# Performance work log

Hardware: AMD Instinct MI355X
Metric: run time of the kernel (lower is better)

## Reference

```python
import jax, jax.numpy as jnp
import numpy as np

B, S_IMG, S_TXT, D, H, HD, R = 1, 1536, 512, 3072, 24, 128, 32
INNER = H * HD  # 3072
EPS = 1e-5


def svdq_linear(x, W, down, up, b=None):
    # Float reference of SVDQW4A4Linear: quantized base GEMM + SVD low-rank branch.
    y = x @ W.T + (x @ down) @ up
    if b is not None:
        y = y + b
    return y


def rms_norm(x, w):
    # RMSNorm over last dim (dim_head)
    var = jnp.mean(x * x, axis=-1, keepdims=True)
    return x * jax.lax.rsqrt(var + EPS) * w


def apply_rope(x, cos, sin):
    # x: (B, S, H, HD); cos/sin: (S, HD//2), interleaved complex rotation
    b, s, h, d = x.shape
    xr = x.reshape(b, s, h, d // 2, 2)
    x0, x1 = xr[..., 0], xr[..., 1]
    c = cos[None, :, None, :]
    sn = sin[None, :, None, :]
    o0 = x0 * c - x1 * sn
    o1 = x0 * sn + x1 * c
    return jnp.stack([o0, o1], axis=-1).reshape(b, s, h, d)


def setup_inputs() -> dict:
    key = jax.random.key(0)
    ks = jax.random.split(key, 24)
    sc = 0.02
    inp = {
        'hidden_states': jax.random.normal(ks[0], (B, S_IMG, D), jnp.float32),
        'encoder_hidden_states': jax.random.normal(ks[1], (B, S_TXT, D), jnp.float32),
    }
    S = S_IMG + S_TXT
    theta = jax.random.uniform(ks[2], (S, HD // 2), jnp.float32, 0.0, 2.0 * np.pi)
    inp['rope_cos'] = jnp.cos(theta)
    inp['rope_sin'] = jnp.sin(theta)
    inp['qkv_w'] = jax.random.normal(ks[3], (3 * INNER, D), jnp.float32) * sc
    inp['qkv_down'] = jax.random.normal(ks[4], (D, R), jnp.float32) * sc
    inp['qkv_up'] = jax.random.normal(ks[5], (R, 3 * INNER), jnp.float32) * sc
    inp['add_qkv_w'] = jax.random.normal(ks[6], (3 * INNER, D), jnp.float32) * sc
    inp['add_qkv_down'] = jax.random.normal(ks[7], (D, R), jnp.float32) * sc
    inp['add_qkv_up'] = jax.random.normal(ks[8], (R, 3 * INNER), jnp.float32) * sc
    inp['out_w'] = jax.random.normal(ks[9], (D, INNER), jnp.float32) * sc
    inp['out_down'] = jax.random.normal(ks[10], (INNER, R), jnp.float32) * sc
    inp['out_up'] = jax.random.normal(ks[11], (R, D), jnp.float32) * sc
    inp['out_b'] = jnp.zeros((D,), jnp.float32)
    inp['add_out_w'] = jax.random.normal(ks[12], (D, INNER), jnp.float32) * sc
    inp['add_out_down'] = jax.random.normal(ks[13], (INNER, R), jnp.float32) * sc
    inp['add_out_up'] = jax.random.normal(ks[14], (R, D), jnp.float32) * sc
    inp['add_out_b'] = jnp.zeros((D,), jnp.float32)
    inp['norm_q_w'] = jnp.ones((HD,), jnp.float32)
    inp['norm_k_w'] = jnp.ones((HD,), jnp.float32)
    inp['norm_added_q_w'] = jnp.ones((HD,), jnp.float32)
    inp['norm_added_k_w'] = jnp.ones((HD,), jnp.float32)
    return inp


def reference(hidden_states, encoder_hidden_states, rope_cos, rope_sin,
              qkv_w, qkv_down, qkv_up,
              add_qkv_w, add_qkv_down, add_qkv_up,
              out_w, out_down, out_up, out_b,
              add_out_w, add_out_down, add_out_up, add_out_b,
              norm_q_w, norm_k_w, norm_added_q_w, norm_added_k_w):
    seq_txt = encoder_hidden_states.shape[1]

    img_qkv = svdq_linear(hidden_states, qkv_w, qkv_down, qkv_up)
    img_q, img_k, img_v = jnp.split(img_qkv, 3, axis=-1)
    txt_qkv = svdq_linear(encoder_hidden_states, add_qkv_w, add_qkv_down, add_qkv_up)
    txt_q, txt_k, txt_v = jnp.split(txt_qkv, 3, axis=-1)

    def heads(x):
        return x.reshape(x.shape[0], x.shape[1], H, HD)

    img_q, img_k, img_v = heads(img_q), heads(img_k), heads(img_v)
    txt_q, txt_k, txt_v = heads(txt_q), heads(txt_k), heads(txt_v)

    img_q = rms_norm(img_q, norm_q_w)
    img_k = rms_norm(img_k, norm_k_w)
    txt_q = rms_norm(txt_q, norm_added_q_w)
    txt_k = rms_norm(txt_k, norm_added_k_w)

    q = jnp.concatenate([txt_q, img_q], axis=1)  # (B, S, H, HD)
    k = jnp.concatenate([txt_k, img_k], axis=1)
    v = jnp.concatenate([txt_v, img_v], axis=1)

    q = apply_rope(q, rope_cos, rope_sin)
    k = apply_rope(k, rope_cos, rope_sin)

    scale = 1.0 / jnp.sqrt(jnp.asarray(HD, q.dtype))
    scores = jnp.einsum('bqhd,bkhd->bhqk', q, k) * scale
    probs = jax.nn.softmax(scores, axis=-1)
    attn = jnp.einsum('bhqk,bkhd->bqhd', probs, v)
    attn = attn.reshape(attn.shape[0], attn.shape[1], INNER)

    txt_attn = attn[:, :seq_txt, :]
    img_attn = attn[:, seq_txt:, :]

    img_out = svdq_linear(img_attn, out_w, out_down, out_up, out_b)
    txt_out = svdq_linear(txt_attn, add_out_w, add_out_down, add_out_up, add_out_b)
    return (img_out, txt_out)
```

## Files before the change

kernel.cpp:

```cpp
#include <hip/hip_runtime.h>
#include <hip/hip_bf16.h>
#include <stdint.h>

typedef __hip_bfloat16 bf16;
typedef __attribute__((ext_vector_type(8))) short short8;
typedef __attribute__((ext_vector_type(4))) short short4b;
typedef __attribute__((ext_vector_type(4))) float floatx4;

__device__ __forceinline__ short bfs(float x) {
    uint32_t u = __builtin_bit_cast(uint32_t, x);
    u += 0x7FFFu + ((u >> 16) & 1u);
    return (short)(u >> 16);
}
__device__ __forceinline__ float b2f(bf16 x) { return __bfloat162float(x); }

__device__ __forceinline__ void load_lds16(const bf16* g, bf16* l) {
    __builtin_amdgcn_global_load_lds(
        (const __attribute__((address_space(1))) uint32_t*)g,
        (__attribute__((address_space(3))) uint32_t*)l, 16, 0, 0);
}

__global__ __launch_bounds__(256) void cvt_bf16(const float* __restrict__ X,
                                                bf16* __restrict__ Y) {
    const size_t i = ((size_t)blockIdx.x * 256 + threadIdx.x) * 8;
    const float4 v0 = *(const float4*)(X + i);
    const float4 v1 = *(const float4*)(X + i + 4);
    short8 o = { bfs(v0.x), bfs(v0.y), bfs(v0.z), bfs(v0.w),
                 bfs(v1.x), bfs(v1.y), bfs(v1.z), bfs(v1.w) };
    *(short8*)(Y + i) = o;
}

__global__ __launch_bounds__(64) void transposeR(const float* __restrict__ U,
                                                 bf16* __restrict__ UT, int N) {
    const int n = blockIdx.x * 64 + threadIdx.x;
    #pragma unroll
    for (int r = 0; r < 32; ++r)
        UT[(size_t)n * 32 + r] = __float2bfloat16(U[(size_t)r * N + n]);
}

__global__ __launch_bounds__(256) void downproj(const bf16* __restrict__ X,
                                                const float* __restrict__ Dn,
                                                bf16* __restrict__ T, int K) {
    const int m = blockIdx.x;
    const int n = threadIdx.x & 31;
    const int kg = threadIdx.x >> 5;
    const bf16* x = X + (size_t)m * K;
    const int kc = K >> 3;
    float acc = 0.f;
    #pragma unroll 4
    for (int k = kg * kc; k < (kg + 1) * kc; ++k)
        acc += b2f(x[k]) * Dn[(size_t)k * 32 + n];
    __shared__ float red[8][32];
    red[kg][n] = acc;
    __syncthreads();
    if (threadIdx.x < 32) {
        float s = 0.f;
        #pragma unroll
        for (int g = 0; g < 8; ++g) s += red[g][n];
        T[(size_t)m * 32 + n] = __float2bfloat16(s);
    }
}

__global__ __launch_bounds__(256) void gemm128(
    const bf16* __restrict__ A, const bf16* __restrict__ B,
    const bf16* __restrict__ T, const bf16* __restrict__ UpT,
    const float* __restrict__ bias, float* __restrict__ C,
    bf16* __restrict__ Qb, bf16* __restrict__ Kb, bf16* __restrict__ Vb,
    int M, int N, int K, int s_base, int mode)
{
    __shared__ __align__(16) bf16 As[128 * 32];
    __shared__ __align__(16) bf16 Bs[128 * 32];
    const int tid = threadIdx.x;
    const int lane = tid & 63, w = tid >> 6;
    const int wm = (w >> 1) * 64, wn = (w & 1) * 64;
    const int lr = lane & 15, lq = lane >> 4;

    int bid = blockIdx.y * gridDim.x + blockIdx.x;
    const int cpx = (gridDim.x * gridDim.y) >> 3;
    bid = (bid & 7) * cpx + (bid >> 3);
    const int by = bid / gridDim.x, bx = bid - by * gridDim.x;
    const int m0 = by * 128, n0 = bx * 128;

    floatx4 acc[4][4] = {};
    const int ksteps = K >> 5;
    for (int kt = 0; kt <= ksteps; ++kt) {
        const bf16 *a_src, *b_src;
        int lda, ldb;
        if (kt < ksteps) {
            a_src = A + (size_t)m0 * K + kt * 32; lda = K;
            b_src = B + (size_t)n0 * K + kt * 32; ldb = K;
        } else {
            a_src = T   + (size_t)m0 * 32; lda = 32;
            b_src = UpT + (size_t)n0 * 32; ldb = 32;
        }
        __syncthreads();
        #pragma unroll
        for (int it = 0; it < 2; ++it) {
            const int c = tid + it * 256;
            const int row = c >> 2, sub = c & 3;
            load_lds16(a_src + (size_t)row * lda + sub * 8, As + c * 8);
        }
        #pragma unroll
        for (int it = 0; it < 2; ++it) {
            const int c = tid + it * 256;
            const int row = c >> 2, sub = c & 3;
            load_lds16(b_src + (size_t)row * ldb + sub * 8, Bs + c * 8);
        }
        __syncthreads();
        short8 af[4], bfr[4];
        #pragma unroll
        for (int i = 0; i < 4; ++i)
            af[i] = *(const short8*)(As + (wm + i * 16 + lr) * 32 + lq * 8);
        #pragma unroll
        for (int j = 0; j < 4; ++j)
            bfr[j] = *(const short8*)(Bs + (wn + j * 16 + lr) * 32 + lq * 8);
        #pragma unroll
        for (int i = 0; i < 4; ++i)
            #pragma unroll
            for (int j = 0; j < 4; ++j)
                acc[i][j] = __builtin_amdgcn_mfma_f32_16x16x32_bf16(
                    af[i], bfr[j], acc[i][j], 0, 0, 0);
    }

    if (mode == 0) {
        #pragma unroll
        for (int j = 0; j < 4; ++j) {
            const int col = n0 + wn + j * 16 + lr;
            const float bv = bias ? bias[col] : 0.0f;
            #pragma unroll
            for (int i = 0; i < 4; ++i) {
                const int rowb = m0 + wm + i * 16 + lq * 4;
                #pragma unroll
                for (int r = 0; r < 4; ++r)
                    C[(size_t)(rowb + r) * N + col] = acc[i][j][r] + bv;
            }
        }
    } else {
        #pragma unroll
        for (int j = 0; j < 4; ++j) {
            const int col = n0 + wn + j * 16 + lr;
            const int which = col / 3072;
            const int cc = col - which * 3072;
            const int hh = cc >> 7, dd = cc & 127;
            #pragma unroll
            for (int i = 0; i < 4; ++i) {
                const int rowb = m0 + wm + i * 16 + lq * 4;
                const int s0 = s_base + rowb;
                if (which == 2) {
                    short4b pv = { bfs(acc[i][j][0]), bfs(acc[i][j][1]),
                                   bfs(acc[i][j][2]), bfs(acc[i][j][3]) };
                    *(short4b*)(Vb + ((size_t)hh * 128 + dd) * 2048 + s0) = pv;
                } else {
                    bf16* dst = (which == 0 ? Qb : Kb)
                              + ((size_t)hh * 2048 + s0) * 128 + dd;
                    #pragma unroll
                    for (int r = 0; r < 4; ++r)
                        dst[(size_t)r * 128] = __float2bfloat16(acc[i][j][r]);
                }
            }
        }
    }
}

__global__ __launch_bounds__(64) void rmsrope(
    bf16* __restrict__ Qb, bf16* __restrict__ Kb,
    const float* __restrict__ cosb, const float* __restrict__ sinb,
    const float* __restrict__ nqw, const float* __restrict__ nkw,
    const float* __restrict__ naqw, const float* __restrict__ nakw)
{
    const int s = blockIdx.x & 2047;
    const int h = blockIdx.x >> 11;
    const int i = threadIdx.x;
    const float c  = cosb[s * 64 + i];
    const float sn = sinb[s * 64 + i];
    const bool txt = (s < 512);
    const size_t base = ((size_t)h * 2048 + s) * 128;

    {
        __hip_bfloat162* row = (__hip_bfloat162*)(Qb + base);
        __hip_bfloat162 pv = row[i];
        float x0 = b2f(pv.x), x1 = b2f(pv.y);
        float ss = x0 * x0 + x1 * x1;
        #pragma unroll
        for (int m = 1; m < 64; m <<= 1) ss += __shfl_xor(ss, m);
        const float rms = rsqrtf(ss * (1.0f / 128.0f) + 1e-5f);
        const float* nw = txt ? naqw : nqw;
        const float y0 = x0 * rms * nw[2 * i];
        const float y1 = x1 * rms * nw[2 * i + 1];
        __hip_bfloat162 o;
        o.x = __float2bfloat16(y0 * c - y1 * sn);
        o.y = __float2bfloat16(y0 * sn + y1 * c);
        row[i] = o;
    }
    {
        __hip_bfloat162* row = (__hip_bfloat162*)(Kb + base);
        __hip_bfloat162 pv = row[i];
        float x0 = b2f(pv.x), x1 = b2f(pv.y);
        float ss = x0 * x0 + x1 * x1;
        #pragma unroll
        for (int m = 1; m < 64; m <<= 1) ss += __shfl_xor(ss, m);
        const float rms = rsqrtf(ss * (1.0f / 128.0f) + 1e-5f);
        const float* nw = txt ? nakw : nkw;
        const float y0 = x0 * rms * nw[2 * i];
        const float y1 = x1 * rms * nw[2 * i + 1];
        __hip_bfloat162 o;
        o.x = __float2bfloat16(y0 * c - y1 * sn);
        o.y = __float2bfloat16(y0 * sn + y1 * c);
        row[i] = o;
    }
}

__global__ __launch_bounds__(256) void attn64(
    const bf16* __restrict__ Qb, const bf16* __restrict__ Kb,
    const bf16* __restrict__ Vb, bf16* __restrict__ attnb)
{
    __shared__ __align__(16) bf16 Ks[64 * 128];
    __shared__ __align__(16) bf16 VsT[128 * 64];
    __shared__ __align__(16) bf16 Ps[4][16 * 64];
    const int tid = threadIdx.x, lane = tid & 63, w = tid >> 6;
    const int lr = lane & 15, lq = lane >> 4;
    const int h = blockIdx.y, q0 = blockIdx.x * 64;
    const float scale = 0.08838834764831845f;

    const bf16* qrow = Qb + ((size_t)h * 2048 + q0 + w * 16 + lr) * 128;
    short8 qf[4];
    #pragma unroll
    for (int ks = 0; ks < 4; ++ks)
        qf[ks] = *(const short8*)(qrow + ks * 32 + lq * 8);

    floatx4 oacc[8] = {};
    float mrow[4] = {-1e30f, -1e30f, -1e30f, -1e30f};
    float lrow[4] = {0.f, 0.f, 0.f, 0.f};

    for (int kt = 0; kt < 32; ++kt) {
        const int kv0 = kt * 64;
        __syncthreads();
        #pragma unroll
        for (int it = 0; it < 4; ++it) {
            const int c = tid + it * 256;
            const int row = c >> 4, cg = (c & 15) ^ (row & 7);
            load_lds16(Kb + ((size_t)h * 2048 + kv0 + row) * 128 + cg * 8,
                       Ks + c * 8);
        }
        #pragma unroll
        for (int it = 0; it < 4; ++it) {
            const int c = tid + it * 256;
            const int row = c >> 3, cg = (c & 7) ^ (row & 7);
            load_lds16(Vb + ((size_t)h * 128 + row) * 2048 + kv0 + cg * 8,
                       VsT + c * 8);
        }
        __syncthreads();

        floatx4 sacc[4] = {};
        __builtin_amdgcn_s_setprio(1);
        #pragma unroll
        for (int ks = 0; ks < 4; ++ks)
            #pragma unroll
            for (int jt = 0; jt < 4; ++jt) {
                const int row = jt * 16 + lr;
                short8 kf = *(const short8*)(
                    Ks + row * 128 + (((ks * 4 + lq) ^ (row & 7)) * 8));
                sacc[jt] = __builtin_amdgcn_mfma_f32_16x16x32_bf16(qf[ks], kf, sacc[jt], 0, 0, 0);
            }
        __builtin_amdgcn_s_setprio(0);

        float alpha_r[4];
        #pragma unroll
        for (int r = 0; r < 4; ++r) {
            float s0 = sacc[0][r] * scale, s1 = sacc[1][r] * scale;
            float s2 = sacc[2][r] * scale, s3 = sacc[3][r] * scale;
            float mx = fmaxf(fmaxf(s0, s1), fmaxf(s2, s3));
            #pragma unroll
            for (int msk = 1; msk < 16; msk <<= 1)
                mx = fmaxf(mx, __shfl_xor(mx, msk));
            const float mn = fmaxf(mrow[r], mx);
            const float al = __expf(mrow[r] - mn);
            s0 = __expf(s0 - mn); s1 = __expf(s1 - mn);
            s2 = __expf(s2 - mn); s3 = __expf(s3 - mn);
            float sum = s0 + s1 + s2 + s3;
            #pragma unroll
            for (int msk = 1; msk < 16; msk <<= 1)
                sum += __shfl_xor(sum, msk);
            lrow[r] = lrow[r] * al + sum;
            mrow[r] = mn;
            alpha_r[r] = al;
            sacc[0][r] = s0; sacc[1][r] = s1; sacc[2][r] = s2; sacc[3][r] = s3;
        }
        #pragma unroll
        for (int nt = 0; nt < 8; ++nt)
            #pragma unroll
            for (int r = 0; r < 4; ++r) oacc[nt][r] *= alpha_r[r];

        #pragma unroll
        for (int jt = 0; jt < 4; ++jt)
            #pragma unroll
            for (int r = 0; r < 4; ++r) {
                const int q = lq * 4 + r;
                const int ir = jt * 16 + lr;
                Ps[w][q * 64 + ((((ir >> 3) ^ (q & 7))) << 3) + (ir & 7)] =
                    __float2bfloat16(sacc[jt][r]);
            }

        short8 pf[2];
        #pragma unroll
        for (int k2 = 0; k2 < 2; ++k2)
            pf[k2] = *(const short8*)(
                &Ps[w][lr * 64 + (((k2 * 4 + lq) ^ (lr & 7)) << 3)]);
        __builtin_amdgcn_s_setprio(1);
        #pragma unroll
        for (int k2 = 0; k2 < 2; ++k2)
            #pragma unroll
            for (int nt = 0; nt < 8; ++nt) {
                const int row = nt * 16 + lr;
                short8 vf = *(const short8*)(
                    VsT + row * 64 + (((k2 * 4 + lq) ^ (row & 7)) * 8));
                oacc[nt] = __builtin_amdgcn_mfma_f32_16x16x32_bf16(pf[k2], vf, oacc[nt], 0, 0, 0);
            }
        __builtin_amdgcn_s_setprio(0);
    }

    float rl[4];
    #pragma unroll
    for (int r = 0; r < 4; ++r) rl[r] = 1.0f / lrow[r];
    #pragma unroll
    for (int nt = 0; nt < 8; ++nt) {
        const int col = h * 128 + nt * 16 + lr;
        #pragma unroll
        for (int r = 0; r < 4; ++r) {
            const int s = q0 + w * 16 + lq * 4 + r;
            attnb[(size_t)s * 3072 + col] = __float2bfloat16(oacc[nt][r] * rl[r]);
        }
    }
}

extern "C" void kernel_launch(void* const* d_in, const int* in_sizes, int n_in,
                              void* d_out, int out_size, void* d_ws, size_t ws_size,
                              hipStream_t stream)
{
    (void)in_sizes; (void)n_in; (void)out_size; (void)ws_size;
    const float* hs        = (const float*)d_in[0];
    const float* ehs       = (const float*)d_in[1];
    const float* rc        = (const float*)d_in[2];
    const float* rs        = (const float*)d_in[3];
    const float* qkv_w     = (const float*)d_in[4];
    const float* qkv_down  = (const float*)d_in[5];
    const float* qkv_up    = (const float*)d_in[6];
    const float* aqkv_w    = (const float*)d_in[7];
    const float* aqkv_down = (const float*)d_in[8];
    const float* aqkv_up   = (const float*)d_in[9];
    const float* out_w     = (const float*)d_in[10];
    const float* out_down  = (const float*)d_in[11];
    const float* out_up    = (const float*)d_in[12];
    const float* out_b     = (const float*)d_in[13];
    const float* aout_w    = (const float*)d_in[14];
    const float* aout_down = (const float*)d_in[15];
    const float* aout_up   = (const float*)d_in[16];
    const float* aout_b    = (const float*)d_in[17];
    const float* nqw  = (const float*)d_in[18];
    const float* nkw  = (const float*)d_in[19];
    const float* naqw = (const float*)d_in[20];
    const float* nakw = (const float*)d_in[21];

    char* ws = (char*)d_ws;
    size_t o = 0;
    bf16* Qb = (bf16*)(ws + o); o += (size_t)24 * 2048 * 128 * 2;
    bf16* Kb = (bf16*)(ws + o); o += (size_t)24 * 2048 * 128 * 2;
    bf16* Vb = (bf16*)(ws + o); o += (size_t)24 * 2048 * 128 * 2;
    bf16* attnb = (bf16*)(ws + o); o += (size_t)2048 * 3072 * 2;
    bf16* Xbi = (bf16*)(ws + o); o += (size_t)1536 * 3072 * 2;
    bf16* Xbt = (bf16*)(ws + o); o += (size_t)512 * 3072 * 2;
    bf16* Wq  = (bf16*)(ws + o); o += (size_t)9216 * 3072 * 2;
    bf16* Waq = (bf16*)(ws + o); o += (size_t)9216 * 3072 * 2;
    bf16* Wo  = Wq;
    bf16* Wao = Wq + (size_t)3072 * 3072;
    bf16* t_img  = (bf16*)(ws + o); o += (size_t)1536 * 32 * 2;
    bf16* t_txt  = (bf16*)(ws + o); o += (size_t)512 * 32 * 2;
    bf16* t2_img = (bf16*)(ws + o); o += (size_t)1536 * 32 * 2;
    bf16* t2_txt = (bf16*)(ws + o); o += (size_t)512 * 32 * 2;
    bf16* upTq  = (bf16*)(ws + o); o += (size_t)9216 * 32 * 2;
    bf16* upTaq = (bf16*)(ws + o); o += (size_t)9216 * 32 * 2;
    bf16* upTo  = (bf16*)(ws + o); o += (size_t)3072 * 32 * 2;
    bf16* upTao = (bf16*)(ws + o); o += (size_t)3072 * 32 * 2;

    cvt_bf16<<<2304, 256, 0, stream>>>(hs, Xbi);
    cvt_bf16<<<768, 256, 0, stream>>>(ehs, Xbt);
    cvt_bf16<<<13824, 256, 0, stream>>>(qkv_w, Wq);
    cvt_bf16<<<13824, 256, 0, stream>>>(aqkv_w, Waq);

    transposeR<<<144, 64, 0, stream>>>(qkv_up, upTq, 9216);
    transposeR<<<144, 64, 0, stream>>>(aqkv_up, upTaq, 9216);
    transposeR<<<48, 64, 0, stream>>>(out_up, upTo, 3072);
    transposeR<<<48, 64, 0, stream>>>(aout_up, upTao, 3072);
    downproj<<<1536, 256, 0, stream>>>(Xbi, qkv_down, t_img, 3072);
    downproj<<<512, 256, 0, stream>>>(Xbt, aqkv_down, t_txt, 3072);

    gemm128<<<dim3(72, 12), 256, 0, stream>>>(Xbi, Wq, t_img, upTq,
        nullptr, nullptr, Qb, Kb, Vb, 1536, 9216, 3072, 512, 1);
    gemm128<<<dim3(72, 4), 256, 0, stream>>>(Xbt, Waq, t_txt, upTaq,
        nullptr, nullptr, Qb, Kb, Vb, 512, 9216, 3072, 0, 1);

    cvt_bf16<<<4608, 256, 0, stream>>>(out_w, Wo);
    cvt_bf16<<<4608, 256, 0, stream>>>(aout_w, Wao);

    rmsrope<<<24 * 2048, 64, 0, stream>>>(Qb, Kb, rc, rs, nqw, nkw, naqw, nakw);

    attn64<<<dim3(32, 24), 256, 0, stream>>>(Qb, Kb, Vb, attnb);

    downproj<<<1536, 256, 0, stream>>>(attnb + (size_t)512 * 3072, out_down, t2_img, 3072);
    downproj<<<512, 256, 0, stream>>>(attnb, aout_down, t2_txt, 3072);

    float* outp = (float*)d_out;
    gemm128<<<dim3(24, 12), 256, 0, stream>>>(attnb + (size_t)512 * 3072, Wo,
        t2_img, upTo, out_b, outp, nullptr, nullptr, nullptr,
        1536, 3072, 3072, 0, 0);
    gemm128<<<dim3(24, 4), 256, 0, stream>>>(attnb, Wao,
        t2_txt, upTao, aout_b, outp + (size_t)1536 * 3072, nullptr, nullptr, nullptr,
        512, 3072, 3072, 0, 0);
}
```

Baseline: 1.104 ms.

## Double-buffer GEMM LDS tiles, merge img/txt GEMM launches, batch rmsrope rows

The GEMM kernel gets two LDS buffers so the global-to-LDS load of the next K step is issued before the MFMAs on the current one, with one barrier per step instead of two. The image and text projections now run as a single grouped launch, with each block picking its operand set by M-tile index, which removes a launch and the tail of the smaller grid. rmsrope packs four rows per 256-thread block and reads the norm weights as float2. The cost is twice the LDS per GEMM block and more pointer-select logic.

Measured after the change: 953.9 us. 1.16x faster.

```diff
diff --git a/kernel.cpp b/kernel.cpp
--- a/kernel.cpp
+++ b/kernel.cpp
@@ -62,14 +62,17 @@
 }
 
 __global__ __launch_bounds__(256) void gemm128(
-    const bf16* __restrict__ A, const bf16* __restrict__ B,
-    const bf16* __restrict__ T, const bf16* __restrict__ UpT,
-    const float* __restrict__ bias, float* __restrict__ C,
+    const bf16* __restrict__ A0, const bf16* __restrict__ B0,
+    const bf16* __restrict__ T0, const bf16* __restrict__ U0,
+    const bf16* __restrict__ A1, const bf16* __restrict__ B1,
+    const bf16* __restrict__ T1, const bf16* __restrict__ U1,
+    const float* __restrict__ bias0, const float* __restrict__ bias1,
+    float* __restrict__ C0, float* __restrict__ C1,
     bf16* __restrict__ Qb, bf16* __restrict__ Kb, bf16* __restrict__ Vb,
-    int M, int N, int K, int s_base, int mode)
+    int mtiles0, int N, int K, int sb0, int sb1, int mode)
 {
-    __shared__ __align__(16) bf16 As[128 * 32];
-    __shared__ __align__(16) bf16 Bs[128 * 32];
+    __shared__ __align__(16) bf16 As[2][128 * 32];
+    __shared__ __align__(16) bf16 Bs[2][128 * 32];
     const int tid = threadIdx.x;
     const int lane = tid & 63, w = tid >> 6;
     const int wm = (w >> 1) * 64, wn = (w & 1) * 64;
@@ -79,60 +82,82 @@
     const int cpx = (gridDim.x * gridDim.y) >> 3;
     bid = (bid & 7) * cpx + (bid >> 3);
     const int by = bid / gridDim.x, bx = bid - by * gridDim.x;
-    const int m0 = by * 128, n0 = bx * 128;
-
-    floatx4 acc[4][4] = {};
+
+    const bool set1 = (by >= mtiles0);
+    const int lby = set1 ? (by - mtiles0) : by;
+    const int m0 = lby * 128, n0 = bx * 128;
+    const bf16* Asel = set1 ? A1 : A0;
+    const bf16* Bsel = set1 ? B1 : B0;
+    const bf16* Tsel = set1 ? T1 : T0;
+    const bf16* Usel = set1 ? U1 : U0;
+    const int s_base = set1 ? sb1 : sb0;
+
     const int ksteps = K >> 5;
-    for (int kt = 0; kt <= ksteps; ++kt) {
+
+    auto stage = [&](int buf, int kt) {
         const bf16 *a_src, *b_src;
         int lda, ldb;
         if (kt < ksteps) {
-            a_src = A + (size_t)m0 * K + kt * 32; lda = K;
-            b_src = B + (size_t)n0 * K + kt * 32; ldb = K;
+            a_src = Asel + (size_t)m0 * K + kt * 32; lda = K;
+            b_src = Bsel + (size_t)n0 * K + kt * 32; ldb = K;
         } else {
-            a_src = T   + (size_t)m0 * 32; lda = 32;
-            b_src = UpT + (size_t)n0 * 32; ldb = 32;
-        }
-        __syncthreads();
+            a_src = Tsel + (size_t)m0 * 32; lda = 32;
+            b_src = Usel + (size_t)n0 * 32; ldb = 32;
+        }
+        bf16* Ad = &As[buf][0];
+        bf16* Bd = &Bs[buf][0];
         #pragma unroll
         for (int it = 0; it < 2; ++it) {
             const int c = tid + it * 256;
             const int row = c >> 2, sub = c & 3;
-            load_lds16(a_src + (size_t)row * lda + sub * 8, As + c * 8);
+            load_lds16(a_src + (size_t)row * lda + sub * 8, Ad + c * 8);
         }
         #pragma unroll
         for (int it = 0; it < 2; ++it) {
             const int c = tid + it * 256;
             const int row = c >> 2, sub = c & 3;
-            load_lds16(b_src + (size_t)row * ldb + sub * 8, Bs + c * 8);
-        }
-        __syncthreads();
+            load_lds16(b_src + (size_t)row * ldb + sub * 8, Bd + c * 8);
+        }
+    };
+
+    floatx4 acc[4][4] = {};
+    stage(0, 0);
+    __syncthreads();
+    int cur = 0;
+    for (int kt = 0; kt <= ksteps; ++kt) {
+        if (kt < ksteps) stage(cur ^ 1, kt + 1);
+        const bf16* Ac = &As[cur][0];
+        const bf16* Bc = &Bs[cur][0];
         short8 af[4], bfr[4];
         #pragma unroll
         for (int i = 0; i < 4; ++i)
-            af[i] = *(const short8*)(As + (wm + i * 16 + lr) * 32 + lq * 8);
+            af[i] = *(const short8*)(Ac + (wm + i * 16 + lr) * 32 + lq * 8);
         #pragma unroll
         for (int j = 0; j < 4; ++j)
-            bfr[j] = *(const short8*)(Bs + (wn + j * 16 + lr) * 32 + lq * 8);
+            bfr[j] = *(const short8*)(Bc + (wn + j * 16 + lr) * 32 + lq * 8);
         #pragma unroll
         for (int i = 0; i < 4; ++i)
             #pragma unroll
             for (int j = 0; j < 4; ++j)
                 acc[i][j] = __builtin_amdgcn_mfma_f32_16x16x32_bf16(
                     af[i], bfr[j], acc[i][j], 0, 0, 0);
+        __syncthreads();
+        cur ^= 1;
     }
 
     if (mode == 0) {
+        float* Csel = set1 ? C1 : C0;
+        const float* bsel = set1 ? bias1 : bias0;
         #pragma unroll
         for (int j = 0; j < 4; ++j) {
             const int col = n0 + wn + j * 16 + lr;
-            const float bv = bias ? bias[col] : 0.0f;
+            const float bv = bsel ? bsel[col] : 0.0f;
             #pragma unroll
             for (int i = 0; i < 4; ++i) {
                 const int rowb = m0 + wm + i * 16 + lq * 4;
                 #pragma unroll
                 for (int r = 0; r < 4; ++r)
-                    C[(size_t)(rowb + r) * N + col] = acc[i][j][r] + bv;
+                    Csel[(size_t)(rowb + r) * N + col] = acc[i][j][r] + bv;
             }
         }
     } else {
@@ -162,15 +187,16 @@
     }
 }
 
-__global__ __launch_bounds__(64) void rmsrope(
+__global__ __launch_bounds__(256) void rmsrope(
     bf16* __restrict__ Qb, bf16* __restrict__ Kb,
     const float* __restrict__ cosb, const float* __restrict__ sinb,
     const float* __restrict__ nqw, const float* __restrict__ nkw,
     const float* __restrict__ naqw, const float* __restrict__ nakw)
 {
-    const int s = blockIdx.x & 2047;
-    const int h = blockIdx.x >> 11;
-    const int i = threadIdx.x;
+    const int idx = blockIdx.x * 4 + (threadIdx.x >> 6);
+    const int i = threadIdx.x & 63;
+    const int s = idx & 2047;
+    const int h = idx >> 11;
     const float c  = cosb[s * 64 + i];
     const float sn = sinb[s * 64 + i];
     const bool txt = (s < 512);
@@ -184,9 +210,9 @@
         #pragma unroll
         for (int m = 1; m < 64; m <<= 1) ss += __shfl_xor(ss, m);
         const float rms = rsqrtf(ss * (1.0f / 128.0f) + 1e-5f);
-        const float* nw = txt ? naqw : nqw;
-        const float y0 = x0 * rms * nw[2 * i];
-        const float y1 = x1 * rms * nw[2 * i + 1];
+        const float2 nw = *(const float2*)((txt ? naqw : nqw) + 2 * i);
+        const float y0 = x0 * rms * nw.x;
+        const float y1 = x1 * rms * nw.y;
         __hip_bfloat162 o;
         o.x = __float2bfloat16(y0 * c - y1 * sn);
         o.y = __float2bfloat16(y0 * sn + y1 * c);
@@ -200,9 +226,9 @@
         #pragma unroll
         for (int m = 1; m < 64; m <<= 1) ss += __shfl_xor(ss, m);
         const float rms = rsqrtf(ss * (1.0f / 128.0f) + 1e-5f);
-        const float* nw = txt ? nakw : nkw;
-        const float y0 = x0 * rms * nw[2 * i];
-        const float y1 = x1 * rms * nw[2 * i + 1];
+        const float2 nw = *(const float2*)((txt ? nakw : nkw) + 2 * i);
+        const float y0 = x0 * rms * nw.x;
+        const float y1 = x1 * rms * nw.y;
         __hip_bfloat162 o;
         o.x = __float2bfloat16(y0 * c - y1 * sn);
         o.y = __float2bfloat16(y0 * sn + y1 * c);
@@ -394,15 +420,16 @@
     downproj<<<1536, 256, 0, stream>>>(Xbi, qkv_down, t_img, 3072);
     downproj<<<512, 256, 0, stream>>>(Xbt, aqkv_down, t_txt, 3072);
 
-    gemm128<<<dim3(72, 12), 256, 0, stream>>>(Xbi, Wq, t_img, upTq,
-        nullptr, nullptr, Qb, Kb, Vb, 1536, 9216, 3072, 512, 1);
-    gemm128<<<dim3(72, 4), 256, 0, stream>>>(Xbt, Waq, t_txt, upTaq,
-        nullptr, nullptr, Qb, Kb, Vb, 512, 9216, 3072, 0, 1);
+    gemm128<<<dim3(72, 16), 256, 0, stream>>>(
+        Xbi, Wq, t_img, upTq,
+        Xbt, Waq, t_txt, upTaq,
+        nullptr, nullptr, nullptr, nullptr,
+        Qb, Kb, Vb, 12, 9216, 3072, 512, 0, 1);
 
     cvt_bf16<<<4608, 256, 0, stream>>>(out_w, Wo);
     cvt_bf16<<<4608, 256, 0, stream>>>(aout_w, Wao);
 
-    rmsrope<<<24 * 2048, 64, 0, stream>>>(Qb, Kb, rc, rs, nqw, nkw, naqw, nakw);
+    rmsrope<<<12288, 256, 0, stream>>>(Qb, Kb, rc, rs, nqw, nkw, naqw, nakw);
 
     attn64<<<dim3(32, 24), 256, 0, stream>>>(Qb, Kb, Vb, attnb);
 
@@ -410,10 +437,9 @@
     downproj<<<512, 256, 0, stream>>>(attnb, aout_down, t2_txt, 3072);
 
     float* outp = (float*)d_out;
-    gemm128<<<dim3(24, 12), 256, 0, stream>>>(attnb + (size_t)512 * 3072, Wo,
-        t2_img, upTo, out_b, outp, nullptr, nullptr, nullptr,
-        1536, 3072, 3072, 0, 0);
-    gemm128<<<dim3(24, 4), 256, 0, stream>>>(attnb, Wao,
-        t2_txt, upTao, aout_b, outp + (size_t)1536 * 3072, nullptr, nullptr, nullptr,
-        512, 3072, 3072, 0, 0);
-}
+    gemm128<<<dim3(24, 16), 256, 0, stream>>>(
+        attnb + (size_t)512 * 3072, Wo, t2_img, upTo,
+        attnb,                      Wao, t2_txt, upTao,
+        out_b, aout_b, outp, outp + (size_t)1536 * 3072,
+        nullptr, nullptr, nullptr, 12, 3072, 3072, 0, 0, 0);
+}
```
